# Performance work log

Measured on AMD Instinct MI355X. Metric: run time of the kernel, lower is better.

The kernel has to match this reference:

```python
import jax, jax.numpy as jnp
import numpy as np

B, N, C = 2, 9216, 512
HEAD, SR = 8, 4
R = 32  # lora rank
SCALING = 4.0 / 32.0  # alpha / r


def setup_inputs() -> dict:
    key = jax.random.key(0)
    ks = jax.random.split(key, 16)
    s = 0.02
    inp = {
        "x": jax.random.normal(ks[0], (B, N, C), jnp.float32),
        "w_q": jax.random.normal(ks[1], (C, C), jnp.float32) * s,
        "b_q": jnp.zeros((C,), jnp.float32),
        "w_kv": jax.random.normal(ks[2], (2 * C, C), jnp.float32) * s,
        "b_kv": jnp.zeros((2 * C,), jnp.float32),
        "w_proj": jax.random.normal(ks[3], (C, C), jnp.float32) * s,
        "b_proj": jnp.zeros((C,), jnp.float32),
        "w_sr": jax.random.normal(ks[4], (C, C, SR, SR), jnp.float32) * s,
        "b_sr": jnp.zeros((C,), jnp.float32),
        "ln_g": jnp.ones((C,), jnp.float32),
        "ln_b": jnp.zeros((C,), jnp.float32),
        "lora_A_q": jax.random.normal(ks[5], (R, C), jnp.float32) * s,
        "lora_B_q": jax.random.normal(ks[6], (C, R), jnp.float32) * s,
        "lora_A_v": jax.random.normal(ks[7], (R, C), jnp.float32) * s,
        "lora_B_v": jax.random.normal(ks[8], (C, R), jnp.float32) * s,
        "H": 96,
        "W": 96,
    }
    return inp


def reference(x, w_q, b_q, w_kv, b_kv, w_proj, b_proj, w_sr, b_sr,
              ln_g, ln_b, lora_A_q, lora_B_q, lora_A_v, lora_B_v, H, W):
    b, n, c = x.shape
    d = c // HEAD
    # q = Linear(x) + LoRA(x) * scaling
    q = x @ w_q.T + b_q + ((x @ lora_A_q.T) @ lora_B_q.T) * SCALING
    q = q.reshape(b, n, HEAD, d).transpose(0, 2, 1, 3)  # (B, h, N, d)
    # spatial reduction: Conv2d(dim, dim, sr, sr) then LayerNorm
    xi = x.transpose(0, 2, 1).reshape(b, c, H, W)
    xs = jax.lax.conv_general_dilated(
        xi, w_sr, window_strides=(SR, SR), padding='VALID',
        dimension_numbers=('NCHW', 'OIHW', 'NCHW'))
    xs = xs + b_sr[None, :, None, None]
    xs = xs.reshape(b, c, -1).transpose(0, 2, 1)  # (B, Nkv, C)
    mu = jnp.mean(xs, axis=-1, keepdims=True)
    var = jnp.var(xs, axis=-1, keepdims=True)
    xs = (xs - mu) * jax.lax.rsqrt(var + 1e-5) * ln_g + ln_b
    # k, v
    kv = (xs @ w_kv.T + b_kv).reshape(b, -1, 2, HEAD, d).transpose(2, 0, 3, 1, 4)
    k, v = kv[0], kv[1]  # (B, h, Nkv, d)
    lv = ((xs @ lora_A_v.T) @ lora_B_v.T) * SCALING  # (B, Nkv, C)
    # faithful to torch: raw memory reshape, NOT a head-transpose
    v = v + lv.reshape(b, HEAD, -1, d)
    # attention
    attn = jax.nn.softmax(jnp.einsum('bhnd,bhmd->bhnm', q, k) * (d ** -0.5), axis=-1)
    out = jnp.einsum('bhnm,bhmd->bhnd', attn, v).transpose(0, 2, 1, 3).reshape(b, n, c)
    return out @ w_proj.T + b_proj
```

## Files before the change

### kernel.cpp

```cpp
#include <hip/hip_runtime.h>

typedef __attribute__((ext_vector_type(8))) __bf16 bf16x8;
typedef __attribute__((ext_vector_type(4))) float f32x4;
typedef __attribute__((ext_vector_type(4))) unsigned int u32x4;
typedef __attribute__((ext_vector_type(2))) unsigned int u32x2;

#define MFMA16(a, b, c) __builtin_amdgcn_mfma_f32_16x16x32_bf16((a), (b), (c), 0, 0, 0)
#define QSCALE 0.18033688011112042f

__device__ __forceinline__ bool input_is_f32(const void* ln_g) {
    return ((const unsigned*)ln_g)[0] == 0x3F800000u;
}

__device__ __forceinline__ float rdf(const void* p, long i, bool f32) {
    return f32 ? ((const float*)p)[i] : (float)((const __bf16*)p)[i];
}

__device__ __forceinline__ void conv_big(const void* s, __bf16* d, long base, bool f) {
    long i = base + (long)threadIdx.x * 8;
    if (f) {
        f32x4 a = ((const f32x4*)s)[i / 4];
        f32x4 b = ((const f32x4*)s)[i / 4 + 1];
        bf16x8 o;
        #pragma unroll
        for (int j = 0; j < 4; ++j) { o[j] = (__bf16)a[j]; o[4 + j] = (__bf16)b[j]; }
        *(bf16x8*)(d + i) = o;
    } else {
        *(u32x4*)(d + i) = ((const u32x4*)s)[i / 8];
    }
}

__device__ __forceinline__ void conv_small(const void* s, __bf16* d, int n, bool f) {
    int i = threadIdx.x * 4;
    if (i < n) {
        #pragma unroll
        for (int j = 0; j < 4; ++j)
            d[i + j] = f ? (__bf16)((const float*)s)[i + j] : ((const __bf16*)s)[i + j];
    }
}

__global__ void convert_prep_kernel(const void* x, const void* w_kv, const void* w_proj,
                                    const void* b_q, const void* b_kv, const void* b_proj,
                                    const void* b_sr, const void* ln_g, const void* ln_b,
                                    const void* __restrict__ w_q,
                                    const void* __restrict__ Aq, const void* __restrict__ Bq,
                                    const void* __restrict__ Av, const void* __restrict__ Bv,
                                    const void* __restrict__ w_sr,
                                    __bf16* x_b, __bf16* w_kv_b, __bf16* w_proj_b,
                                    __bf16* b_q_b, __bf16* b_kv_b, __bf16* b_proj_b,
                                    __bf16* b_sr_b, __bf16* ln_g_b, __bf16* ln_b_b,
                                    __bf16* __restrict__ w_q_eff, __bf16* __restrict__ w_lv,
                                    __bf16* __restrict__ w_sr_t) {
    const bool f = input_is_f32(ln_g);
    int blk = blockIdx.x;
    if (blk < 4608)      conv_big(x, x_b, (long)blk * 2048, f);
    else if (blk < 4864) conv_big(w_kv, w_kv_b, (long)(blk - 4608) * 2048, f);
    else if (blk < 4992) conv_big(w_proj, w_proj_b, (long)(blk - 4864) * 2048, f);
    else if (blk == 4992) conv_small(b_q, b_q_b, 512, f);
    else if (blk == 4993) conv_small(b_kv, b_kv_b, 1024, f);
    else if (blk == 4994) conv_small(b_proj, b_proj_b, 512, f);
    else if (blk == 4995) conv_small(b_sr, b_sr_b, 512, f);
    else if (blk == 4996) conv_small(ln_g, ln_g_b, 512, f);
    else if (blk == 4997) conv_small(ln_b, ln_b_b, 512, f);
    else {
        int tid = (blk - 4998) * 256 + threadIdx.x;
        if (tid < 262144) {
            int o = tid >> 9, c = tid & 511;
            float acc = 0.f;
            #pragma unroll 8
            for (int r = 0; r < 32; ++r)
                acc += rdf(Bq, o * 32 + r, f) * rdf(Aq, r * 512 + c, f);
            w_q_eff[tid] = (__bf16)(rdf(w_q, tid, f) + 0.125f * acc);
        } else if (tid < 524288) {
            int t = tid - 262144;
            int o = t >> 9, c = t & 511;
            float acc = 0.f;
            #pragma unroll 8
            for (int r = 0; r < 32; ++r)
                acc += rdf(Bv, o * 32 + r, f) * rdf(Av, r * 512 + c, f);
            w_lv[t] = (__bf16)(0.125f * acc);
        } else if (tid < 786432) {
            int t = tid - 524288;
            int o = t >> 9, i = t & 511;
            #pragma unroll
            for (int p = 0; p < 16; ++p)
                w_sr_t[(size_t)o * 8192 + p * 512 + i] = (__bf16)rdf(w_sr, (long)t * 16 + p, f);
        }
    }
}

__global__ __launch_bounds__(256) void gemm128(const __bf16* __restrict__ A,
                                               const __bf16* __restrict__ Bt,
                                               const __bf16* __restrict__ bias,
                                               void* __restrict__ out, int mode) {
    __shared__ __attribute__((aligned(16))) char lds[36864];
    char* As = lds;
    char* Bs = lds + 18432;
    const int tid = threadIdx.x;
    const int m0 = blockIdx.x << 7, n0 = blockIdx.y << 7;
    const int w = tid >> 6, lane = tid & 63;
    const int wm = (w >> 1) << 6, wn = (w & 1) << 6;
    const int lr = lane & 15, lg = lane >> 4;

    f32x4 acc[4][4] = {};

    const int srow = tid >> 1;
    const int half = tid & 1;
    const __bf16* Arow = A + (size_t)(m0 + srow) * 512 + half * 32;
    const __bf16* Brow = Bt + (size_t)(n0 + srow) * 512 + half * 32;
    char* Asw = As + srow * 144 + half * 64;
    char* Bsw = Bs + srow * 144 + half * 64;

    for (int k0 = 0; k0 < 512; k0 += 64) {
        u32x4 a0 = *(const u32x4*)(Arow + k0);
        u32x4 a1 = *(const u32x4*)(Arow + k0 + 8);
        u32x4 a2 = *(const u32x4*)(Arow + k0 + 16);
        u32x4 a3 = *(const u32x4*)(Arow + k0 + 24);
        u32x4 b0 = *(const u32x4*)(Brow + k0);
        u32x4 b1 = *(const u32x4*)(Brow + k0 + 8);
        u32x4 b2 = *(const u32x4*)(Brow + k0 + 16);
        u32x4 b3 = *(const u32x4*)(Brow + k0 + 24);
        __syncthreads();
        *(u32x4*)(Asw) = a0;
        *(u32x4*)(Asw + 16) = a1;
        *(u32x4*)(Asw + 32) = a2;
        *(u32x4*)(Asw + 48) = a3;
        *(u32x4*)(Bsw) = b0;
        *(u32x4*)(Bsw + 16) = b1;
        *(u32x4*)(Bsw + 32) = b2;
        *(u32x4*)(Bsw + 48) = b3;
        __syncthreads();
        bf16x8 a[4][2], b[4][2];
        #pragma unroll
        for (int i = 0; i < 4; ++i)
            #pragma unroll
            for (int ks = 0; ks < 2; ++ks)
                a[i][ks] = *(const bf16x8*)(As + (wm + i * 16 + lr) * 144 + ks * 64 + lg * 16);
        #pragma unroll
        for (int j = 0; j < 4; ++j)
            #pragma unroll
            for (int ks = 0; ks < 2; ++ks)
                b[j][ks] = *(const bf16x8*)(Bs + (wn + j * 16 + lr) * 144 + ks * 64 + lg * 16);
        #pragma unroll
        for (int i = 0; i < 4; ++i)
            #pragma unroll
            for (int j = 0; j < 4; ++j)
                #pragma unroll
                for (int ks = 0; ks < 2; ++ks)
                    acc[i][j] = MFMA16(a[i][ks], b[j][ks], acc[i][j]);
    }

    #pragma unroll
    for (int j = 0; j < 4; ++j) {
        int col = n0 + wn + j * 16 + lr;
        float bv = (float)bias[col];
        #pragma unroll
        for (int i = 0; i < 4; ++i) {
            int rb = m0 + wm + i * 16 + lg * 4;
            #pragma unroll
            for (int r = 0; r < 4; ++r) {
                float v = acc[i][j][r] + bv;
                int grow = rb + r;
                if (mode == 0) {
                    ((float*)out)[(size_t)grow * 512 + col] = v;
                } else {
                    int b_ = grow >= 9216 ? 1 : 0;
                    int nn = grow - b_ * 9216;
                    ((__bf16*)out)[(((size_t)(b_ * 8 + (col >> 6))) * 9216 + nn) * 64 +
                                   (col & 63)] = (__bf16)(v * QSCALE);
                }
            }
        }
    }
}

__global__ __launch_bounds__(256) void conv_gemm(const __bf16* __restrict__ x,
                                                 const __bf16* __restrict__ Wt,
                                                 float* __restrict__ part) {
    __shared__ __attribute__((aligned(16))) char lds[18432];
    char* As = lds;
    char* Bs = lds + 9216;
    const int tid = threadIdx.x;
    const int m0 = blockIdx.x << 6, n0 = blockIdx.y << 6;
    const int kz = blockIdx.z;
    const int kbase = kz << 10;
    const int w = tid >> 6, lane = tid & 63;
    const int wm = (w >> 1) << 5, wn = (w & 1) << 5;
    const int lr = lane & 15, lg = lane >> 4;

    const int srow = tid >> 2, sc = tid & 3;
    int m = m0 + srow;
    int bb = m >= 576 ? 1 : 0;
    int rem = m - bb * 576;
    int oy = rem / 24;
    int ox = rem - oy * 24;
    const __bf16* xrow = x + ((size_t)bb * 9216 + oy * 384 + ox * 4) * 512;
    const __bf16* brow = Wt + (size_t)(n0 + srow) * 8192;

    f32x4 acc[2][2] = {};
    for (int kk = 0; kk < 1024; kk += 64) {
        int k0 = kbase + kk;
        int p = k0 >> 9;
        int i0 = k0 & 511;
        int ky = p >> 2, kx = p & 3;
        const __bf16* xsrc = xrow + ((ky * 96 + kx) << 9) + i0;
        __syncthreads();
        #pragma unroll
        for (int j = 0; j < 2; ++j) {
            int c = sc + j * 4;
            u32x4 av = *(const u32x4*)(xsrc + c * 8);
            u32x4 bv = *(const u32x4*)(brow + k0 + c * 8);
            *(u32x4*)(As + srow * 144 + c * 16) = av;
            *(u32x4*)(Bs + srow * 144 + c * 16) = bv;
        }
        __syncthreads();
        bf16x8 a[2][2], b[2][2];
        #pragma unroll
        for (int i = 0; i < 2; ++i)
            #pragma unroll
            for (int ks = 0; ks < 2; ++ks) {
                a[i][ks] = *(const bf16x8*)(As + (wm + i * 16 + lr) * 144 + ks * 64 + lg * 16);
                b[i][ks] = *(const bf16x8*)(Bs + (wn + i * 16 + lr) * 144 + ks * 64 + lg * 16);
            }
        #pragma unroll
        for (int i = 0; i < 2; ++i)
            #pragma unroll
            for (int j = 0; j < 2; ++j)
                #pragma unroll
                for (int ks = 0; ks < 2; ++ks)
                    acc[i][j] = MFMA16(a[i][ks], b[j][ks], acc[i][j]);
    }
    float* pout = part + (size_t)kz * 589824;
    #pragma unroll
    for (int j = 0; j < 2; ++j) {
        int col = n0 + wn + j * 16 + lr;
        #pragma unroll
        for (int i = 0; i < 2; ++i) {
            int rb = m0 + wm + i * 16 + lg * 4;
            #pragma unroll
            for (int r = 0; r < 4; ++r)
                pout[(size_t)(rb + r) * 512 + col] = acc[i][j][r];
        }
    }
}

__global__ __launch_bounds__(64) void lnorm(const float* __restrict__ parts,
                                            const __bf16* __restrict__ b_sr,
                                            const __bf16* __restrict__ g,
                                            const __bf16* __restrict__ be,
                                            __bf16* __restrict__ out) {
    int row = blockIdx.x;
    int lane = threadIdx.x;
    const float* xr = parts + (size_t)row * 512;
    float v[8], s = 0.f, sq = 0.f;
    #pragma unroll
    for (int i = 0; i < 8; ++i) {
        int c = lane + i * 64;
        float t = (float)b_sr[c];
        #pragma unroll
        for (int sp = 0; sp < 8; ++sp)
            t += xr[(size_t)sp * 589824 + c];
        v[i] = t;
        s += t;
        sq += t * t;
    }
    #pragma unroll
    for (int d = 1; d < 64; d <<= 1) {
        s += __shfl_xor(s, d);
        sq += __shfl_xor(sq, d);
    }
    float mean = s * (1.0f / 512.0f);
    float var = sq * (1.0f / 512.0f) - mean * mean;
    float rstd = rsqrtf(var + 1e-5f);
    __bf16* orow = out + (size_t)row * 512;
    #pragma unroll
    for (int i = 0; i < 8; ++i) {
        int c = lane + i * 64;
        orow[c] = (__bf16)((v[i] - mean) * rstd * (float)g[c] + (float)be[c]);
    }
}

__global__ __launch_bounds__(256) void kv_gemm(const __bf16* __restrict__ xs,
                                               const __bf16* __restrict__ w_kv,
                                               const __bf16* __restrict__ w_lv,
                                               const __bf16* __restrict__ b_kv,
                                               __bf16* __restrict__ k_t,
                                               float* __restrict__ v_raw,
                                               __bf16* __restrict__ lv) {
    __shared__ __attribute__((aligned(16))) char lds[18432];
    char* As = lds;
    char* Bs = lds + 9216;
    const int tid = threadIdx.x;
    const int m0 = blockIdx.x << 6, n0 = blockIdx.y << 6;
    const int w = tid >> 6, lane = tid & 63;
    const int wm = (w >> 1) << 5, wn = (w & 1) << 5;
    const int lr = lane & 15, lg = lane >> 4;

    const int srow = tid >> 2, sc = tid & 3;
    const __bf16* arow = xs + (size_t)(m0 + srow) * 512;
    const __bf16* brow = (n0 < 1024) ? (w_kv + (size_t)(n0 + srow) * 512)
                                     : (w_lv + (size_t)(n0 - 1024 + srow) * 512);

    f32x4 acc[2][2] = {};
    for (int k0 = 0; k0 < 512; k0 += 64) {
        __syncthreads();
        #pragma unroll
        for (int j = 0; j < 2; ++j) {
            int c = sc + j * 4;
            u32x4 av = *(const u32x4*)(arow + k0 + c * 8);
            u32x4 bv = *(const u32x4*)(brow + k0 + c * 8);
            *(u32x4*)(As + srow * 144 + c * 16) = av;
            *(u32x4*)(Bs + srow * 144 + c * 16) = bv;
        }
        __syncthreads();
        bf16x8 a[2][2], b[2][2];
        #pragma unroll
        for (int i = 0; i < 2; ++i)
            #pragma unroll
            for (int ks = 0; ks < 2; ++ks) {
                a[i][ks] = *(const bf16x8*)(As + (wm + i * 16 + lr) * 144 + ks * 64 + lg * 16);
                b[i][ks] = *(const bf16x8*)(Bs + (wn + i * 16 + lr) * 144 + ks * 64 + lg * 16);
            }
        #pragma unroll
        for (int i = 0; i < 2; ++i)
            #pragma unroll
            for (int j = 0; j < 2; ++j)
                #pragma unroll
                for (int ks = 0; ks < 2; ++ks)
                    acc[i][j] = MFMA16(a[i][ks], b[j][ks], acc[i][j]);
    }
    #pragma unroll
    for (int j = 0; j < 2; ++j) {
        int col = n0 + wn + j * 16 + lr;
        float bv = (col < 1024) ? (float)b_kv[col] : 0.0f;
        #pragma unroll
        for (int i = 0; i < 2; ++i) {
            int rb = m0 + wm + i * 16 + lg * 4;
            #pragma unroll
            for (int r = 0; r < 4; ++r) {
                int grow = rb + r;
                float val = acc[i][j][r] + bv;
                int b_ = grow >= 576 ? 1 : 0;
                int mm = grow - b_ * 576;
                if (col < 512) {
                    int h = col >> 6, dd = col & 63;
                    k_t[(((size_t)(b_ * 8 + h)) * 576 + mm) * 64 + dd] = (__bf16)val;
                } else if (col < 1024) {
                    v_raw[((size_t)b_ * 576 + mm) * 512 + (col - 512)] = val;
                } else {
                    lv[((size_t)b_ * 576 + mm) * 512 + (col - 1024)] = (__bf16)val;
                }
            }
        }
    }
}

__global__ void v_fixup(const float* __restrict__ v_raw, const __bf16* __restrict__ lv,
                        __bf16* __restrict__ vT) {
    int tid = blockIdx.x * 256 + threadIdx.x;
    if (tid >= 589824) return;
    int mm = tid % 576;
    int rest = tid / 576;
    int dd = rest & 63;
    int bh = rest >> 6;
    int b_ = bh >> 3, h = bh & 7;
    int flat = h * 36864 + mm * 64 + dd;
    int n2 = flat >> 9, c2 = flat & 511;
    float val = v_raw[((size_t)b_ * 576 + mm) * 512 + h * 64 + dd] +
                (float)lv[((size_t)b_ * 576 + n2) * 512 + c2];
    vT[tid] = (__bf16)val;
}

__global__ __launch_bounds__(128, 2) void attn_kernel(const __bf16* __restrict__ q_t,
                                                      const __bf16* __restrict__ k_t,
                                                      const __bf16* __restrict__ vT,
                                                      __bf16* __restrict__ attnv) {
    __shared__ __attribute__((aligned(16))) char lds[18432];
    char* Ks = lds;
    char* Vs = lds + 9216;
    const int tid = threadIdx.x;
    const int w = tid >> 6, lane = tid & 63;
    const int lr = lane & 15, lg = lane >> 4;
    const int bh = blockIdx.y;
    const int qrow0 = (blockIdx.x << 7) + (w << 6);

    bf16x8 qf[4][2];
    #pragma unroll
    for (int qb = 0; qb < 4; ++qb)
        #pragma unroll
        for (int ks = 0; ks < 2; ++ks)
            qf[qb][ks] = *(const bf16x8*)(q_t + ((size_t)bh * 9216 + qrow0 + qb * 16 + lr) * 64 +
                                          ks * 32 + lg * 8);

    bf16x8 ones;
    #pragma unroll
    for (int j = 0; j < 8; ++j) ones[j] = (__bf16)1.0f;

    f32x4 oacc[4][4] = {};
    f32x4 lacc[4] = {};

    const int rr = tid >> 1, hc = tid & 1;
    const __bf16* kg = k_t + ((size_t)bh * 576 + rr) * 64 + hc * 32;
    char* ksw = Ks + rr * 144 + hc * 64;
    const __bf16* vg = vT + ((size_t)bh * 64 + rr) * 576 + hc * 32;
    char* vsw = Vs + rr * 144;

    for (int kv0 = 0; kv0 < 576; kv0 += 64) {
        u32x4 k0v = *(const u32x4*)(kg + (size_t)kv0 * 64);
        u32x4 k1v = *(const u32x4*)(kg + (size_t)kv0 * 64 + 8);
        u32x4 k2v = *(const u32x4*)(kg + (size_t)kv0 * 64 + 16);
        u32x4 k3v = *(const u32x4*)(kg + (size_t)kv0 * 64 + 24);
        u32x4 v0v = *(const u32x4*)(vg + kv0);
        u32x4 v1v = *(const u32x4*)(vg + kv0 + 8);
        u32x4 v2v = *(const u32x4*)(vg + kv0 + 16);
        u32x4 v3v = *(const u32x4*)(vg + kv0 + 24);
        __syncthreads();
        *(u32x4*)(ksw) = k0v;
        *(u32x4*)(ksw + 16) = k1v;
        *(u32x4*)(ksw + 32) = k2v;
        *(u32x4*)(ksw + 48) = k3v;
        {
            u32x2 t0, t1, t2, t3;
            t0[0] = v0v[0]; t0[1] = v0v[1];
            t1[0] = v0v[2]; t1[1] = v0v[3];
            t2[0] = v1v[0]; t2[1] = v1v[1];
            t3[0] = v1v[2]; t3[1] = v1v[3];
            char* p = vsw + (hc << 6);
            *(u32x2*)(p) = t0;
            *(u32x2*)(p + 16) = t1;
            *(u32x2*)(p + 32) = t2;
            *(u32x2*)(p + 48) = t3;
            t0[0] = v2v[0]; t0[1] = v2v[1];
            t1[0] = v2v[2]; t1[1] = v2v[3];
            t2[0] = v3v[0]; t2[1] = v3v[1];
            t3[0] = v3v[2]; t3[1] = v3v[3];
            p += 8;
            *(u32x2*)(p) = t0;
            *(u32x2*)(p + 16) = t1;
            *(u32x2*)(p + 32) = t2;
            *(u32x2*)(p + 48) = t3;
        }
        __syncthreads();

        #pragma unroll
        for (int ch = 0; ch < 2; ++ch) {
            bf16x8 kf[2][2];
            #pragma unroll
            for (int kb = 0; kb < 2; ++kb)
                #pragma unroll
                for (int ks = 0; ks < 2; ++ks)
                    kf[kb][ks] = *(const bf16x8*)(Ks + ((ch * 2 + kb) * 16 + lr) * 144 +
                                                  ks * 64 + lg * 16);
            f32x4 st[2][4] = {};
            #pragma unroll
            for (int kb = 0; kb < 2; ++kb)
                #pragma unroll
                for (int qb = 0; qb < 4; ++qb)
                    #pragma unroll
                    for (int ks = 0; ks < 2; ++ks)
                        st[kb][qb] = MFMA16(kf[kb][ks], qf[qb][ks], st[kb][qb]);
            bf16x8 vf[4];
            #pragma unroll
            for (int nd = 0; nd < 4; ++nd)
                vf[nd] = *(const bf16x8*)(Vs + (nd * 16 + lr) * 144 + ch * 64 + lg * 16);
            #pragma unroll
            for (int qb = 0; qb < 4; ++qb) {
                bf16x8 pa;
                #pragma unroll
                for (int kb = 0; kb < 2; ++kb)
                    #pragma unroll
                    for (int r = 0; r < 4; ++r)
                        pa[kb * 4 + r] = (__bf16)__builtin_amdgcn_exp2f(st[kb][qb][r]);
                #pragma unroll
                for (int nd = 0; nd < 4; ++nd)
                    oacc[qb][nd] = MFMA16(pa, vf[nd], oacc[qb][nd]);
                lacc[qb] = MFMA16(pa, ones, lacc[qb]);
            }
        }
    }

    const int b_ = bh >> 3, h = bh & 7;
    #pragma unroll
    for (int qb = 0; qb < 4; ++qb) {
        f32x4 linv;
        #pragma unroll
        for (int r = 0; r < 4; ++r) linv[r] = 1.0f / lacc[qb][r];
        #pragma unroll
        for (int nd = 0; nd < 4; ++nd)
            #pragma unroll
            for (int r = 0; r < 4; ++r) {
                int row = qrow0 + qb * 16 + lg * 4 + r;
                int col = h * 64 + nd * 16 + lr;
                attnv[((size_t)b_ * 9216 + row) * 512 + col] =
                    (__bf16)(oacc[qb][nd][r] * linv[r]);
            }
    }
}

extern "C" void kernel_launch(void* const* d_in, const int* in_sizes, int n_in,
                              void* d_out, int out_size, void* d_ws, size_t ws_size,
                              hipStream_t stream) {
    const void* x      = d_in[0];
    const void* w_q    = d_in[1];
    const void* b_q    = d_in[2];
    const void* w_kv   = d_in[3];
    const void* b_kv   = d_in[4];
    const void* w_proj = d_in[5];
    const void* b_proj = d_in[6];
    const void* w_sr   = d_in[7];
    const void* b_sr   = d_in[8];
    const void* ln_g   = d_in[9];
    const void* ln_b   = d_in[10];
    const void* A_q    = d_in[11];
    const void* B_q    = d_in[12];
    const void* A_v    = d_in[13];
    const void* B_v    = d_in[14];

    char* ws = (char*)d_ws;
    __bf16* x_b      = (__bf16*)(ws);
    __bf16* attnv    = (__bf16*)(ws);
    float*  parts    = (float*)(ws + 18874368);
    __bf16* q_t      = (__bf16*)(ws + 18874368);
    __bf16* k_t      = (__bf16*)(ws + 37748736);
    __bf16* vT       = (__bf16*)(ws + 38928384);
    __bf16* w_q_eff  = (__bf16*)(ws + 40108032);
    __bf16* w_lv     = (__bf16*)(ws + 40632320);
    __bf16* w_sr_t   = (__bf16*)(ws + 41156608);
    __bf16* w_kv_b   = (__bf16*)(ws + 49545216);
    __bf16* w_proj_b = (__bf16*)(ws + 50593792);
    __bf16* xs_ln    = (__bf16*)(ws + 53477376);
    float*  v_raw    = (float*)(ws + 54657024);
    __bf16* lv       = (__bf16*)(ws + 57016320);
    __bf16* b_q_b    = (__bf16*)(ws + 58195968);
    __bf16* b_kv_b   = (__bf16*)(ws + 58196992);
    __bf16* b_proj_b = (__bf16*)(ws + 58199040);
    __bf16* b_sr_b   = (__bf16*)(ws + 58200064);
    __bf16* ln_g_b   = (__bf16*)(ws + 58201088);
    __bf16* ln_b_b   = (__bf16*)(ws + 58202112);

    convert_prep_kernel<<<8070, 256, 0, stream>>>(
        x, w_kv, w_proj, b_q, b_kv, b_proj, b_sr, ln_g, ln_b,
        w_q, A_q, B_q, A_v, B_v, w_sr,
        x_b, w_kv_b, w_proj_b, b_q_b, b_kv_b, b_proj_b, b_sr_b, ln_g_b, ln_b_b,
        w_q_eff, w_lv, w_sr_t);
    conv_gemm<<<dim3(18, 8, 8), 256, 0, stream>>>(x_b, w_sr_t, parts);
    lnorm<<<1152, 64, 0, stream>>>(parts, b_sr_b, ln_g_b, ln_b_b, xs_ln);
    gemm128<<<dim3(144, 4), 256, 0, stream>>>(x_b, w_q_eff, b_q_b, q_t, 1);
    kv_gemm<<<dim3(18, 24), 256, 0, stream>>>(xs_ln, w_kv_b, w_lv, b_kv_b, k_t, v_raw, lv);
    v_fixup<<<2304, 256, 0, stream>>>(v_raw, lv, vT);
    attn_kernel<<<dim3(72, 16), 128, 0, stream>>>(q_t, k_t, vT, attnv);
    gemm128<<<dim3(144, 4), 256, 0, stream>>>(attnv, w_proj_b, b_proj_b, d_out, 0);
}
```

Baseline: 267.7 us.

## Prefetch next K tile in GEMMs and attention, retile conv GEMM and attention blocks

Adds register prefetching of the next K-slice global loads after the LDS barrier in gemm128, kv_gemm, conv_gemm and attn_kernel, so global latency overlaps the MFMA work. conv_gemm moves to 128x128 tiles with 16 split-K slices (one per kernel tap), and lnorm now sums 16 partials. The partials buffer moves to a separate workspace region. Attention blocks go from 128 to 256 threads, covering 256 query rows per block with smaller per-thread K/V staging. More split-K partial traffic and higher register pressure are the risks.

```diff
diff --git a/kernel.cpp b/kernel.cpp
--- a/kernel.cpp
+++ b/kernel.cpp
@@ -89,10 +89,10 @@
     }
 }
 
-__global__ __launch_bounds__(256) void gemm128(const __bf16* __restrict__ A,
-                                               const __bf16* __restrict__ Bt,
-                                               const __bf16* __restrict__ bias,
-                                               void* __restrict__ out, int mode) {
+__global__ __launch_bounds__(256, 2) void gemm128(const __bf16* __restrict__ A,
+                                                  const __bf16* __restrict__ Bt,
+                                                  const __bf16* __restrict__ bias,
+                                                  void* __restrict__ out, int mode) {
     __shared__ __attribute__((aligned(16))) char lds[36864];
     char* As = lds;
     char* Bs = lds + 18432;
@@ -111,15 +111,16 @@
     char* Asw = As + srow * 144 + half * 64;
     char* Bsw = Bs + srow * 144 + half * 64;
 
+    u32x4 a0 = *(const u32x4*)(Arow);
+    u32x4 a1 = *(const u32x4*)(Arow + 8);
+    u32x4 a2 = *(const u32x4*)(Arow + 16);
+    u32x4 a3 = *(const u32x4*)(Arow + 24);
+    u32x4 b0 = *(const u32x4*)(Brow);
+    u32x4 b1 = *(const u32x4*)(Brow + 8);
+    u32x4 b2 = *(const u32x4*)(Brow + 16);
+    u32x4 b3 = *(const u32x4*)(Brow + 24);
+
     for (int k0 = 0; k0 < 512; k0 += 64) {
-        u32x4 a0 = *(const u32x4*)(Arow + k0);
-        u32x4 a1 = *(const u32x4*)(Arow + k0 + 8);
-        u32x4 a2 = *(const u32x4*)(Arow + k0 + 16);
-        u32x4 a3 = *(const u32x4*)(Arow + k0 + 24);
-        u32x4 b0 = *(const u32x4*)(Brow + k0);
-        u32x4 b1 = *(const u32x4*)(Brow + k0 + 8);
-        u32x4 b2 = *(const u32x4*)(Brow + k0 + 16);
-        u32x4 b3 = *(const u32x4*)(Brow + k0 + 24);
         __syncthreads();
         *(u32x4*)(Asw) = a0;
         *(u32x4*)(Asw + 16) = a1;
@@ -130,6 +131,17 @@
         *(u32x4*)(Bsw + 32) = b2;
         *(u32x4*)(Bsw + 48) = b3;
         __syncthreads();
+        int kn = k0 + 64;
+        if (kn < 512) {
+            a0 = *(const u32x4*)(Arow + kn);
+            a1 = *(const u32x4*)(Arow + kn + 8);
+            a2 = *(const u32x4*)(Arow + kn + 16);
+            a3 = *(const u32x4*)(Arow + kn + 24);
+            b0 = *(const u32x4*)(Brow + kn);
+            b1 = *(const u32x4*)(Brow + kn + 8);
+            b2 = *(const u32x4*)(Brow + kn + 16);
+            b3 = *(const u32x4*)(Brow + kn + 24);
+        }
         bf16x8 a[4][2], b[4][2];
         #pragma unroll
         for (int i = 0; i < 4; ++i)
@@ -174,68 +186,92 @@
     }
 }
 
-__global__ __launch_bounds__(256) void conv_gemm(const __bf16* __restrict__ x,
-                                                 const __bf16* __restrict__ Wt,
-                                                 float* __restrict__ part) {
-    __shared__ __attribute__((aligned(16))) char lds[18432];
+__global__ __launch_bounds__(256, 2) void conv_gemm(const __bf16* __restrict__ x,
+                                                    const __bf16* __restrict__ Wt,
+                                                    float* __restrict__ part) {
+    __shared__ __attribute__((aligned(16))) char lds[36864];
     char* As = lds;
-    char* Bs = lds + 9216;
+    char* Bs = lds + 18432;
     const int tid = threadIdx.x;
-    const int m0 = blockIdx.x << 6, n0 = blockIdx.y << 6;
+    const int m0 = blockIdx.x << 7, n0 = blockIdx.y << 7;
     const int kz = blockIdx.z;
-    const int kbase = kz << 10;
     const int w = tid >> 6, lane = tid & 63;
-    const int wm = (w >> 1) << 5, wn = (w & 1) << 5;
+    const int wm = (w >> 1) << 6, wn = (w & 1) << 6;
     const int lr = lane & 15, lg = lane >> 4;
 
-    const int srow = tid >> 2, sc = tid & 3;
+    f32x4 acc[4][4] = {};
+
+    const int srow = tid >> 1;
+    const int half = tid & 1;
     int m = m0 + srow;
     int bb = m >= 576 ? 1 : 0;
     int rem = m - bb * 576;
     int oy = rem / 24;
     int ox = rem - oy * 24;
-    const __bf16* xrow = x + ((size_t)bb * 9216 + oy * 384 + ox * 4) * 512;
-    const __bf16* brow = Wt + (size_t)(n0 + srow) * 8192;
-
-    f32x4 acc[2][2] = {};
-    for (int kk = 0; kk < 1024; kk += 64) {
-        int k0 = kbase + kk;
-        int p = k0 >> 9;
-        int i0 = k0 & 511;
-        int ky = p >> 2, kx = p & 3;
-        const __bf16* xsrc = xrow + ((ky * 96 + kx) << 9) + i0;
-        __syncthreads();
-        #pragma unroll
-        for (int j = 0; j < 2; ++j) {
-            int c = sc + j * 4;
-            u32x4 av = *(const u32x4*)(xsrc + c * 8);
-            u32x4 bv = *(const u32x4*)(brow + k0 + c * 8);
-            *(u32x4*)(As + srow * 144 + c * 16) = av;
-            *(u32x4*)(Bs + srow * 144 + c * 16) = bv;
-        }
-        __syncthreads();
-        bf16x8 a[2][2], b[2][2];
-        #pragma unroll
-        for (int i = 0; i < 2; ++i)
-            #pragma unroll
-            for (int ks = 0; ks < 2; ++ks) {
+    int ky = kz >> 2, kx = kz & 3;
+    const __bf16* Arow = x + ((size_t)bb * 9216 + (size_t)(oy * 384 + ky * 96 + ox * 4 + kx)) * 512
+                         + half * 32;
+    const __bf16* Brow = Wt + (size_t)(n0 + srow) * 8192 + kz * 512 + half * 32;
+    char* Asw = As + srow * 144 + half * 64;
+    char* Bsw = Bs + srow * 144 + half * 64;
+
+    u32x4 a0 = *(const u32x4*)(Arow);
+    u32x4 a1 = *(const u32x4*)(Arow + 8);
+    u32x4 a2 = *(const u32x4*)(Arow + 16);
+    u32x4 a3 = *(const u32x4*)(Arow + 24);
+    u32x4 b0 = *(const u32x4*)(Brow);
+    u32x4 b1 = *(const u32x4*)(Brow + 8);
+    u32x4 b2 = *(const u32x4*)(Brow + 16);
+    u32x4 b3 = *(const u32x4*)(Brow + 24);
+
+    for (int k0 = 0; k0 < 512; k0 += 64) {
+        __syncthreads();
+        *(u32x4*)(Asw) = a0;
+        *(u32x4*)(Asw + 16) = a1;
+        *(u32x4*)(Asw + 32) = a2;
+        *(u32x4*)(Asw + 48) = a3;
+        *(u32x4*)(Bsw) = b0;
+        *(u32x4*)(Bsw + 16) = b1;
+        *(u32x4*)(Bsw + 32) = b2;
+        *(u32x4*)(Bsw + 48) = b3;
+        __syncthreads();
+        int kn = k0 + 64;
+        if (kn < 512) {
+            a0 = *(const u32x4*)(Arow + kn);
+            a1 = *(const u32x4*)(Arow + kn + 8);
+            a2 = *(const u32x4*)(Arow + kn + 16);
+            a3 = *(const u32x4*)(Arow + kn + 24);
+            b0 = *(const u32x4*)(Brow + kn);
+            b1 = *(const u32x4*)(Brow + kn + 8);
+            b2 = *(const u32x4*)(Brow + kn + 16);
+            b3 = *(const u32x4*)(Brow + kn + 24);
+        }
+        bf16x8 a[4][2], b[4][2];
+        #pragma unroll
+        for (int i = 0; i < 4; ++i)
+            #pragma unroll
+            for (int ks = 0; ks < 2; ++ks)
                 a[i][ks] = *(const bf16x8*)(As + (wm + i * 16 + lr) * 144 + ks * 64 + lg * 16);
-                b[i][ks] = *(const bf16x8*)(Bs + (wn + i * 16 + lr) * 144 + ks * 64 + lg * 16);
-            }
-        #pragma unroll
-        for (int i = 0; i < 2; ++i)
-            #pragma unroll
-            for (int j = 0; j < 2; ++j)
+        #pragma unroll
+        for (int j = 0; j < 4; ++j)
+            #pragma unroll
+            for (int ks = 0; ks < 2; ++ks)
+                b[j][ks] = *(const bf16x8*)(Bs + (wn + j * 16 + lr) * 144 + ks * 64 + lg * 16);
+        #pragma unroll
+        for (int i = 0; i < 4; ++i)
+            #pragma unroll
+            for (int j = 0; j < 4; ++j)
                 #pragma unroll
                 for (int ks = 0; ks < 2; ++ks)
                     acc[i][j] = MFMA16(a[i][ks], b[j][ks], acc[i][j]);
     }
+
     float* pout = part + (size_t)kz * 589824;
     #pragma unroll
-    for (int j = 0; j < 2; ++j) {
+    for (int j = 0; j < 4; ++j) {
         int col = n0 + wn + j * 16 + lr;
         #pragma unroll
-        for (int i = 0; i < 2; ++i) {
+        for (int i = 0; i < 4; ++i) {
             int rb = m0 + wm + i * 16 + lg * 4;
             #pragma unroll
             for (int r = 0; r < 4; ++r)
@@ -258,7 +294,7 @@
         int c = lane + i * 64;
         float t = (float)b_sr[c];
         #pragma unroll
-        for (int sp = 0; sp < 8; ++sp)
+        for (int sp = 0; sp < 16; ++sp)
             t += xr[(size_t)sp * 589824 + c];
         v[i] = t;
         s += t;
@@ -301,18 +337,33 @@
     const __bf16* brow = (n0 < 1024) ? (w_kv + (size_t)(n0 + srow) * 512)
                                      : (w_lv + (size_t)(n0 - 1024 + srow) * 512);
 
+    u32x4 pav[2], pbv[2];
+    #pragma unroll
+    for (int j = 0; j < 2; ++j) {
+        int c = sc + j * 4;
+        pav[j] = *(const u32x4*)(arow + c * 8);
+        pbv[j] = *(const u32x4*)(brow + c * 8);
+    }
+
     f32x4 acc[2][2] = {};
     for (int k0 = 0; k0 < 512; k0 += 64) {
         __syncthreads();
         #pragma unroll
         for (int j = 0; j < 2; ++j) {
             int c = sc + j * 4;
-            u32x4 av = *(const u32x4*)(arow + k0 + c * 8);
-            u32x4 bv = *(const u32x4*)(brow + k0 + c * 8);
-            *(u32x4*)(As + srow * 144 + c * 16) = av;
-            *(u32x4*)(Bs + srow * 144 + c * 16) = bv;
-        }
-        __syncthreads();
+            *(u32x4*)(As + srow * 144 + c * 16) = pav[j];
+            *(u32x4*)(Bs + srow * 144 + c * 16) = pbv[j];
+        }
+        __syncthreads();
+        int kn = k0 + 64;
+        if (kn < 512) {
+            #pragma unroll
+            for (int j = 0; j < 2; ++j) {
+                int c = sc + j * 4;
+                pav[j] = *(const u32x4*)(arow + kn + c * 8);
+                pbv[j] = *(const u32x4*)(brow + kn + c * 8);
+            }
+        }
         bf16x8 a[2][2], b[2][2];
         #pragma unroll
         for (int i = 0; i < 2; ++i)
@@ -371,7 +422,7 @@
     vT[tid] = (__bf16)val;
 }
 
-__global__ __launch_bounds__(128, 2) void attn_kernel(const __bf16* __restrict__ q_t,
+__global__ __launch_bounds__(256, 2) void attn_kernel(const __bf16* __restrict__ q_t,
                                                       const __bf16* __restrict__ k_t,
                                                       const __bf16* __restrict__ vT,
                                                       __bf16* __restrict__ attnv) {
@@ -382,7 +433,7 @@
     const int w = tid >> 6, lane = tid & 63;
     const int lr = lane & 15, lg = lane >> 4;
     const int bh = blockIdx.y;
-    const int qrow0 = (blockIdx.x << 7) + (w << 6);
+    const int qrow0 = (blockIdx.x << 8) + (w << 6);
 
     bf16x8 qf[4][2];
     #pragma unroll
@@ -399,48 +450,41 @@
     f32x4 oacc[4][4] = {};
     f32x4 lacc[4] = {};
 
-    const int rr = tid >> 1, hc = tid & 1;
-    const __bf16* kg = k_t + ((size_t)bh * 576 + rr) * 64 + hc * 32;
-    char* ksw = Ks + rr * 144 + hc * 64;
-    const __bf16* vg = vT + ((size_t)bh * 64 + rr) * 576 + hc * 32;
+    const int rr = tid >> 2, q4 = tid & 3;
+    const __bf16* kg = k_t + ((size_t)bh * 576 + rr) * 64 + q4 * 16;
+    char* ksw = Ks + rr * 144 + q4 * 32;
+    const __bf16* vg = vT + ((size_t)bh * 64 + rr) * 576 + q4 * 16;
     char* vsw = Vs + rr * 144;
+    const int offA = ((q4 & 1) << 3) | ((q4 >> 1) << 6);
+
+    u32x4 k0v = *(const u32x4*)(kg);
+    u32x4 k1v = *(const u32x4*)(kg + 8);
+    u32x4 v0v = *(const u32x4*)(vg);
+    u32x4 v1v = *(const u32x4*)(vg + 8);
 
     for (int kv0 = 0; kv0 < 576; kv0 += 64) {
-        u32x4 k0v = *(const u32x4*)(kg + (size_t)kv0 * 64);
-        u32x4 k1v = *(const u32x4*)(kg + (size_t)kv0 * 64 + 8);
-        u32x4 k2v = *(const u32x4*)(kg + (size_t)kv0 * 64 + 16);
-        u32x4 k3v = *(const u32x4*)(kg + (size_t)kv0 * 64 + 24);
-        u32x4 v0v = *(const u32x4*)(vg + kv0);
-        u32x4 v1v = *(const u32x4*)(vg + kv0 + 8);
-        u32x4 v2v = *(const u32x4*)(vg + kv0 + 16);
-        u32x4 v3v = *(const u32x4*)(vg + kv0 + 24);
         __syncthreads();
         *(u32x4*)(ksw) = k0v;
         *(u32x4*)(ksw + 16) = k1v;
-        *(u32x4*)(ksw + 32) = k2v;
-        *(u32x4*)(ksw + 48) = k3v;
         {
             u32x2 t0, t1, t2, t3;
             t0[0] = v0v[0]; t0[1] = v0v[1];
             t1[0] = v0v[2]; t1[1] = v0v[3];
             t2[0] = v1v[0]; t2[1] = v1v[1];
             t3[0] = v1v[2]; t3[1] = v1v[3];
-            char* p = vsw + (hc << 6);
-            *(u32x2*)(p) = t0;
-            *(u32x2*)(p + 16) = t1;
-            *(u32x2*)(p + 32) = t2;
-            *(u32x2*)(p + 48) = t3;
-            t0[0] = v2v[0]; t0[1] = v2v[1];
-            t1[0] = v2v[2]; t1[1] = v2v[3];
-            t2[0] = v3v[0]; t2[1] = v3v[1];
-            t3[0] = v3v[2]; t3[1] = v3v[3];
-            p += 8;
-            *(u32x2*)(p) = t0;
-            *(u32x2*)(p + 16) = t1;
-            *(u32x2*)(p + 32) = t2;
-            *(u32x2*)(p + 48) = t3;
-        }
-        __syncthreads();
+            *(u32x2*)(vsw + offA) = t0;
+            *(u32x2*)(vsw + offA + 16) = t1;
+            *(u32x2*)(vsw + offA + 32) = t2;
+            *(u32x2*)(vsw + offA + 48) = t3;
+        }
+        __syncthreads();
+        int kvn = kv0 + 64;
+        if (kvn < 576) {
+            k0v = *(const u32x4*)(kg + (size_t)kvn * 64);
+            k1v = *(const u32x4*)(kg + (size_t)kvn * 64 + 8);
+            v0v = *(const u32x4*)(vg + kvn);
+            v1v = *(const u32x4*)(vg + kvn + 8);
+        }
 
         #pragma unroll
         for (int ch = 0; ch < 2; ++ch) {
@@ -519,7 +563,6 @@
     char* ws = (char*)d_ws;
     __bf16* x_b      = (__bf16*)(ws);
     __bf16* attnv    = (__bf16*)(ws);
-    float*  parts    = (float*)(ws + 18874368);
     __bf16* q_t      = (__bf16*)(ws + 18874368);
     __bf16* k_t      = (__bf16*)(ws + 37748736);
     __bf16* vT       = (__bf16*)(ws + 38928384);
@@ -537,17 +580,18 @@
     __bf16* b_sr_b   = (__bf16*)(ws + 58200064);
     __bf16* ln_g_b   = (__bf16*)(ws + 58201088);
     __bf16* ln_b_b   = (__bf16*)(ws + 58202112);
+    float*  parts    = (float*)(ws + 58204160);
 
     convert_prep_kernel<<<8070, 256, 0, stream>>>(
         x, w_kv, w_proj, b_q, b_kv, b_proj, b_sr, ln_g, ln_b,
         w_q, A_q, B_q, A_v, B_v, w_sr,
         x_b, w_kv_b, w_proj_b, b_q_b, b_kv_b, b_proj_b, b_sr_b, ln_g_b, ln_b_b,
         w_q_eff, w_lv, w_sr_t);
-    conv_gemm<<<dim3(18, 8, 8), 256, 0, stream>>>(x_b, w_sr_t, parts);
+    conv_gemm<<<dim3(9, 4, 16), 256, 0, stream>>>(x_b, w_sr_t, parts);
     lnorm<<<1152, 64, 0, stream>>>(parts, b_sr_b, ln_g_b, ln_b_b, xs_ln);
     gemm128<<<dim3(144, 4), 256, 0, stream>>>(x_b, w_q_eff, b_q_b, q_t, 1);
     kv_gemm<<<dim3(18, 24), 256, 0, stream>>>(xs_ln, w_kv_b, w_lv, b_kv_b, k_t, v_raw, lv);
     v_fixup<<<2304, 256, 0, stream>>>(v_raw, lv, vT);
-    attn_kernel<<<dim3(72, 16), 128, 0, stream>>>(q_t, k_t, vT, attnv);
+    attn_kernel<<<dim3(36, 16), 256, 0, stream>>>(q_t, k_t, vT, attnv);
     gemm128<<<dim3(144, 4), 256, 0, stream>>>(attnv, w_proj_b, b_proj_b, d_out, 0);
 }
```

Result: slower. 273.3 us (+2.1%).
